# Kernel tuning notes

Hardware: AMD Instinct MI355X
Metric: run time of the kernel (lower is better)

Reference implementation:

```python
import jax, jax.numpy as jnp
import numpy as np

EPS = 1e-5

def _proj(x, W, g, b, m, v):
    # 1x1 conv (no bias) + BatchNorm2d (inference stats) + ReLU
    y = jnp.einsum('bchw,oc->bohw', x, W)
    scale = g / jnp.sqrt(v + EPS)
    y = y * scale[:, None, None] + (b - m * scale)[:, None, None]
    return jax.nn.relu(y)

def setup_inputs() -> dict:
    key = jax.random.key(0)
    B, C, H, W = 4, 192, 64, 64
    ks = jax.random.split(key, 10)
    d = {
        'lr_hsi': jax.random.normal(ks[0], (B, C, H, W), jnp.float32),
        'refine_hsi': jax.random.normal(ks[1], (B, C, H, W), jnp.float32),
    }
    for i, name in enumerate(['q', 'k', 'v', 't']):
        d['W' + name] = jax.random.normal(ks[2 + i], (C, C), jnp.float32) * 0.05
        d['g' + name] = jnp.ones((C,), jnp.float32)
        d['b' + name] = jnp.zeros((C,), jnp.float32)
        d['m' + name] = jnp.zeros((C,), jnp.float32)
        d['v' + name] = jnp.ones((C,), jnp.float32)
    return d

def reference(lr_hsi, refine_hsi,
              Wq, gq, bq, mq, vq,
              Wk, gk, bk, mk, vk,
              Wv, gv, bv, mv, vv,
              Wt, gt, bt, mt, vt):
    B, C, H, W = refine_hsi.shape
    HW = H * W
    q = _proj(refine_hsi, Wq, gq, bq, mq, vq).reshape(B, C, HW).transpose(0, 2, 1)  # [B, HWq, C]
    k = _proj(lr_hsi, Wk, gk, bk, mk, vk).reshape(B, C, HW)                          # [B, C, HWk]
    v = _proj(lr_hsi, Wv, gv, bv, mv, vv).reshape(B, C, HW).transpose(0, 2, 1)      # [B, HWk, C]
    corr = jnp.einsum('bqc,bck->bqk', q, k) * (C ** -0.5)  # [B, HWq, HWk]
    corr = jax.nn.softmax(corr, axis=1)  # NOTE: softmax over the QUERY axis (dim=1), as in source
    ss = jnp.einsum('bqk,bkc->bqc', corr, v)               # [B, HWq, C]
    ss = ss.transpose(0, 2, 1).reshape(B, C, H, W)
    out = _proj(ss, Wt, gt, bt, mt, vt)
    return (out, corr)
```

## Files before the change

### kernel.cpp

```cpp
#include <hip/hip_runtime.h>
#include <math.h>

typedef __attribute__((ext_vector_type(4))) float f32x4;
typedef __attribute__((ext_vector_type(8))) short bf16x8;

__device__ __forceinline__ unsigned short f2bf(float f) {
  unsigned int u = __builtin_bit_cast(unsigned int, f);
  u += 0x7FFFu + ((u >> 16) & 1u);
  return (unsigned short)(u >> 16);
}

__device__ __forceinline__ f32x4 mfma16(bf16x8 a, bf16x8 b, f32x4 c) {
  return __builtin_amdgcn_mfma_f32_16x16x32_bf16(a, b, c, 0, 0, 0);
}

__global__ void prep_kernel(const float* __restrict__ W, const float* __restrict__ g,
                            const float* __restrict__ bb, const float* __restrict__ mm,
                            const float* __restrict__ vv,
                            unsigned short* __restrict__ Wout, float* __restrict__ bout,
                            float alpha) {
  int idx = blockIdx.x * 256 + threadIdx.x;
  if (idx < 192 * 192) {
    int o = idx / 192;
    float s = g[o] * rsqrtf(vv[o] + 1e-5f);
    Wout[idx] = f2bf(W[idx] * s * alpha);
  }
  if (idx < 192) {
    float s = g[idx] * rsqrtf(vv[idx] + 1e-5f);
    bout[idx] = (bb[idx] - mm[idx] * s) * alpha;
  }
}

template <int LAYOUT, bool F32OUT>
__launch_bounds__(256)
__global__ void proj_kernel(const float* __restrict__ X,
                            const unsigned short* __restrict__ Wp,
                            const float* __restrict__ bias,
                            void* __restrict__ Yv) {
  const int o0 = blockIdx.x * 64;
  const int hw0 = blockIdx.y * 64;
  const int b = blockIdx.z;
  const int w = threadIdx.x >> 6, l = threadIdx.x & 63;
  const int l16 = l & 15, lg = l >> 4;
  const float* Xb = X + (size_t)b * 192 * 4096;

  f32x4 acc[4] = {f32x4{0,0,0,0}, f32x4{0,0,0,0}, f32x4{0,0,0,0}, f32x4{0,0,0,0}};

  for (int ks = 0; ks < 6; ++ks) {
    const int c0 = ks * 32 + lg * 8;
    bf16x8 a = *(const bf16x8*)(Wp + (size_t)(o0 + 16 * w + l16) * 192 + c0);
#pragma unroll
    for (int n = 0; n < 4; ++n) {
      const int hw = hw0 + 16 * n + l16;
      bf16x8 bfr;
#pragma unroll
      for (int j = 0; j < 8; ++j)
        bfr[j] = (short)f2bf(Xb[(size_t)(c0 + j) * 4096 + hw]);
      acc[n] = mfma16(a, bfr, acc[n]);
    }
  }

#pragma unroll
  for (int n = 0; n < 4; ++n) {
    const int hw = hw0 + 16 * n + l16;
    float vv4[4];
#pragma unroll
    for (int r = 0; r < 4; ++r) {
      const int o = o0 + 16 * w + lg * 4 + r;
      vv4[r] = fmaxf(acc[n][r] + bias[o], 0.0f);
    }
    if (LAYOUT == 1) {
      unsigned int lo = (unsigned)f2bf(vv4[0]) | ((unsigned)f2bf(vv4[1]) << 16);
      unsigned int hi = (unsigned)f2bf(vv4[2]) | ((unsigned)f2bf(vv4[3]) << 16);
      uint2 pk; pk.x = lo; pk.y = hi;
      *(uint2*)((unsigned short*)Yv + ((size_t)b * 4096 + hw) * 192 + o0 + 16 * w + lg * 4) = pk;
    } else {
#pragma unroll
      for (int r = 0; r < 4; ++r) {
        const int o = o0 + 16 * w + lg * 4 + r;
        if (F32OUT)
          ((float*)Yv)[((size_t)b * 192 + o) * 4096 + hw] = vv4[r];
        else
          ((unsigned short*)Yv)[((size_t)b * 192 + o) * 4096 + hw] = f2bf(vv4[r]);
      }
    }
  }
}

__launch_bounds__(256)
__global__ void pass1_kernel(const unsigned short* __restrict__ qp,
                             const unsigned short* __restrict__ kpT,
                             float* __restrict__ colsum) {
  const int q0 = blockIdx.x * 128, k0 = blockIdx.y * 128, b = blockIdx.z;
  const int w = threadIdx.x >> 6, l = threadIdx.x & 63;
  const int l16 = l & 15, lg = l >> 4;
  const unsigned short* qb = qp + (size_t)b * 4096 * 192;
  const unsigned short* kb = kpT + (size_t)b * 4096 * 192;

  __shared__ __align__(16) unsigned short kpl[128][200];
  __shared__ float cs[4][128];

  {
    const int t = threadIdx.x;
#pragma unroll
    for (int i = 0; i < 12; ++i) {
      int idx = t + i * 256;
      int row = idx / 24, cu = idx % 24;
      uint4 vdat = *(const uint4*)(kb + (size_t)(k0 + row) * 192 + cu * 8);
      *(uint4*)&kpl[row][cu * 8] = vdat;
    }
  }
  __syncthreads();

  f32x4 acc[2][8];
#pragma unroll
  for (int m = 0; m < 2; ++m)
#pragma unroll
    for (int n = 0; n < 8; ++n) acc[m][n] = f32x4{0, 0, 0, 0};

  for (int ks = 0; ks < 6; ++ks) {
    const int c0 = ks * 32 + lg * 8;
    bf16x8 a0 = *(const bf16x8*)(qb + (size_t)(q0 + 32 * w + l16) * 192 + c0);
    bf16x8 a1 = *(const bf16x8*)(qb + (size_t)(q0 + 32 * w + 16 + l16) * 192 + c0);
#pragma unroll
    for (int n = 0; n < 8; ++n) {
      bf16x8 bfr = *(const bf16x8*)&kpl[16 * n + l16][c0];
      acc[0][n] = mfma16(a0, bfr, acc[0][n]);
      acc[1][n] = mfma16(a1, bfr, acc[1][n]);
    }
  }

  float part[8];
#pragma unroll
  for (int n = 0; n < 8; ++n) {
    float s = 0.f;
#pragma unroll
    for (int r = 0; r < 4; ++r)
      s += __builtin_amdgcn_exp2f(acc[0][n][r]) + __builtin_amdgcn_exp2f(acc[1][n][r]);
    s += __shfl_xor(s, 16);
    s += __shfl_xor(s, 32);
    part[n] = s;
  }
  if (l < 16) {
#pragma unroll
    for (int n = 0; n < 8; ++n) cs[w][16 * n + l] = part[n];
  }
  __syncthreads();
  const int t = threadIdx.x;
  if (t < 128) {
    float s = cs[0][t] + cs[1][t] + cs[2][t] + cs[3][t];
    atomicAdd(&colsum[(size_t)b * 4096 + k0 + t], s);
  }
}

__global__ void invert_kernel(float* __restrict__ p, int n) {
  int i = blockIdx.x * 256 + threadIdx.x;
  if (i < n) p[i] = 1.0f / p[i];
}

__launch_bounds__(512)
__global__ void pass2_kernel(const unsigned short* __restrict__ qp,
                             const unsigned short* __restrict__ kpT,
                             const unsigned short* __restrict__ vpN,
                             const float* __restrict__ rcol,
                             float* __restrict__ corr,
                             float* __restrict__ ssN) {
  const int q0 = blockIdx.x * 64;
  const int b = blockIdx.y;
  const int w = threadIdx.x >> 6, l = threadIdx.x & 63;
  const int l16 = l & 15, lg = l >> 4;
  const int mw = w & 1, nw = w >> 1;
  const unsigned short* qb = qp + (size_t)b * 4096 * 192;
  const unsigned short* kb = kpT + (size_t)b * 4096 * 192;
  const unsigned short* vb = vpN + (size_t)b * 192 * 4096;
  const float* rc = rcol + (size_t)b * 4096;
  float* corb = corr + (size_t)b * 4096 * 4096;

  __shared__ __align__(16) float cor[64][132];

  bf16x8 af[2][6];
#pragma unroll
  for (int tm = 0; tm < 2; ++tm)
#pragma unroll
    for (int ks = 0; ks < 6; ++ks)
      af[tm][ks] = *(const bf16x8*)(qb + (size_t)(q0 + 16 * (2 * mw + tm) + l16) * 192 + ks * 32 + lg * 8);

  f32x4 ssa[2][3];
#pragma unroll
  for (int tm = 0; tm < 2; ++tm)
#pragma unroll
    for (int j = 0; j < 3; ++j) ssa[tm][j] = f32x4{0, 0, 0, 0};

  for (int kc = 0; kc < 32; ++kc) {
    const int k0 = kc * 128;
    f32x4 sa[2][2];
#pragma unroll
    for (int tm = 0; tm < 2; ++tm)
#pragma unroll
      for (int tn = 0; tn < 2; ++tn) sa[tm][tn] = f32x4{0, 0, 0, 0};

    for (int ks = 0; ks < 6; ++ks) {
      const int c0 = ks * 32 + lg * 8;
#pragma unroll
      for (int tn = 0; tn < 2; ++tn) {
        const int kcol = k0 + 16 * (2 * nw + tn) + l16;
        bf16x8 bfr = *(const bf16x8*)(kb + (size_t)kcol * 192 + c0);
        sa[0][tn] = mfma16(af[0][ks], bfr, sa[0][tn]);
        sa[1][tn] = mfma16(af[1][ks], bfr, sa[1][tn]);
      }
    }
    float rcv[2];
#pragma unroll
    for (int tn = 0; tn < 2; ++tn) rcv[tn] = rc[k0 + 16 * (2 * nw + tn) + l16];
#pragma unroll
    for (int tm = 0; tm < 2; ++tm)
#pragma unroll
      for (int tn = 0; tn < 2; ++tn)
#pragma unroll
        for (int r = 0; r < 4; ++r)
          sa[tm][tn][r] = __builtin_amdgcn_exp2f(sa[tm][tn][r]) * rcv[tn];

    __syncthreads();
#pragma unroll
    for (int tm = 0; tm < 2; ++tm)
#pragma unroll
      for (int tn = 0; tn < 2; ++tn) {
        const int col = 16 * (2 * nw + tn) + l16;
#pragma unroll
        for (int r = 0; r < 4; ++r)
          cor[16 * (2 * mw + tm) + lg * 4 + r][col] = sa[tm][tn][r];
      }
    __syncthreads();

    {
      const int t = threadIdx.x;
#pragma unroll
      for (int it = 0; it < 4; ++it) {
        int idx = t + it * 512;
        int row = idx >> 5, seg = idx & 31;
        f32x4 v4 = *(const f32x4*)&cor[row][seg * 4];
        *(f32x4*)(corb + (size_t)(q0 + row) * 4096 + k0 + seg * 4) = v4;
      }
    }

#pragma unroll
    for (int ks2 = 0; ks2 < 4; ++ks2) {
      const int cc = ks2 * 32 + lg * 8;
      bf16x8 pa[2];
#pragma unroll
      for (int tm = 0; tm < 2; ++tm) {
        f32x4 p0 = *(const f32x4*)&cor[16 * (2 * mw + tm) + l16][cc];
        f32x4 p1 = *(const f32x4*)&cor[16 * (2 * mw + tm) + l16][cc + 4];
#pragma unroll
        for (int j = 0; j < 4; ++j) {
          pa[tm][j] = (short)f2bf(p0[j]);
          pa[tm][j + 4] = (short)f2bf(p1[j]);
        }
      }
#pragma unroll
      for (int j = 0; j < 3; ++j) {
        const int ccol = 16 * (nw + 4 * j) + l16;
        bf16x8 bfr = *(const bf16x8*)(vb + (size_t)ccol * 4096 + k0 + cc);
        ssa[0][j] = mfma16(pa[0], bfr, ssa[0][j]);
        ssa[1][j] = mfma16(pa[1], bfr, ssa[1][j]);
      }
    }
  }

#pragma unroll
  for (int tm = 0; tm < 2; ++tm)
#pragma unroll
    for (int j = 0; j < 3; ++j) {
      const int ccol = 16 * (nw + 4 * j) + l16;
#pragma unroll
      for (int r = 0; r < 4; ++r) {
        const int qrow = q0 + 16 * (2 * mw + tm) + lg * 4 + r;
        ssN[((size_t)b * 192 + ccol) * 4096 + qrow] = ssa[tm][j][r];
      }
    }
}

extern "C" void kernel_launch(void* const* d_in, const int* in_sizes, int n_in,
                              void* d_out, int out_size, void* d_ws, size_t ws_size,
                              hipStream_t stream) {
  (void)in_sizes; (void)n_in; (void)out_size; (void)ws_size;
  const float* lr = (const float*)d_in[0];
  const float* refine = (const float*)d_in[1];

  char* ws = (char*)d_ws;
  unsigned short* w4 = (unsigned short*)(ws + 0);
  float* bias4 = (float*)(ws + 294912);
  unsigned short* qp = (unsigned short*)(ws + 297984);
  unsigned short* kp = (unsigned short*)(ws + 297984 + 6291456);
  unsigned short* vp = (unsigned short*)(ws + 297984 + 2 * 6291456);
  float* colsum = (float*)(ws + 297984 + 3 * 6291456);
  float* ssN = (float*)(ws + 297984 + 3 * 6291456 + 65536);

  float* out0 = (float*)d_out;
  float* corr = out0 + 3145728;

  const float alpha = (float)(1.4426950408889634 / sqrt(192.0));

  for (int p = 0; p < 4; ++p) {
    prep_kernel<<<dim3(144), dim3(256), 0, stream>>>(
        (const float*)d_in[2 + 5 * p], (const float*)d_in[3 + 5 * p],
        (const float*)d_in[4 + 5 * p], (const float*)d_in[5 + 5 * p],
        (const float*)d_in[6 + 5 * p],
        w4 + p * 36864, bias4 + p * 192, p == 0 ? alpha : 1.0f);
  }
  hipMemsetAsync(colsum, 0, 65536, stream);

  proj_kernel<1, false><<<dim3(3, 64, 4), dim3(256), 0, stream>>>(refine, w4, bias4, qp);
  proj_kernel<1, false><<<dim3(3, 64, 4), dim3(256), 0, stream>>>(lr, w4 + 36864, bias4 + 192, kp);
  proj_kernel<0, false><<<dim3(3, 64, 4), dim3(256), 0, stream>>>(lr, w4 + 2 * 36864, bias4 + 2 * 192, vp);

  pass1_kernel<<<dim3(32, 32, 4), dim3(256), 0, stream>>>(qp, kp, colsum);
  invert_kernel<<<dim3(64), dim3(256), 0, stream>>>(colsum, 16384);
  pass2_kernel<<<dim3(64, 4), dim3(512), 0, stream>>>(qp, kp, vp, colsum, corr, ssN);

  proj_kernel<0, true><<<dim3(3, 64, 4), dim3(256), 0, stream>>>(ssN, w4 + 3 * 36864, bias4 + 3 * 192, out0);
}
```

Before: 312.9 us.

## Split pass2 key range across two blocks and sum partials in final projection

```diff
diff --git a/kernel.cpp b/kernel.cpp
--- a/kernel.cpp
+++ b/kernel.cpp
@@ -31,12 +31,12 @@
   }
 }
 
-template <int LAYOUT, bool F32OUT>
+template <int LAYOUT>
 __launch_bounds__(256)
 __global__ void proj_kernel(const float* __restrict__ X,
                             const unsigned short* __restrict__ Wp,
                             const float* __restrict__ bias,
-                            void* __restrict__ Yv) {
+                            unsigned short* __restrict__ Yv) {
   const int o0 = blockIdx.x * 64;
   const int hw0 = blockIdx.y * 64;
   const int b = blockIdx.z;
@@ -73,16 +73,59 @@
       unsigned int lo = (unsigned)f2bf(vv4[0]) | ((unsigned)f2bf(vv4[1]) << 16);
       unsigned int hi = (unsigned)f2bf(vv4[2]) | ((unsigned)f2bf(vv4[3]) << 16);
       uint2 pk; pk.x = lo; pk.y = hi;
-      *(uint2*)((unsigned short*)Yv + ((size_t)b * 4096 + hw) * 192 + o0 + 16 * w + lg * 4) = pk;
+      *(uint2*)(Yv + ((size_t)b * 4096 + hw) * 192 + o0 + 16 * w + lg * 4) = pk;
     } else {
 #pragma unroll
       for (int r = 0; r < 4; ++r) {
         const int o = o0 + 16 * w + lg * 4 + r;
-        if (F32OUT)
-          ((float*)Yv)[((size_t)b * 192 + o) * 4096 + hw] = vv4[r];
-        else
-          ((unsigned short*)Yv)[((size_t)b * 192 + o) * 4096 + hw] = f2bf(vv4[r]);
-      }
+        Yv[((size_t)b * 192 + o) * 4096 + hw] = f2bf(vv4[r]);
+      }
+    }
+  }
+}
+
+template <int NS>
+__launch_bounds__(256)
+__global__ void proj_sum_kernel(const float* __restrict__ X,
+                                const unsigned short* __restrict__ Wp,
+                                const float* __restrict__ bias,
+                                float* __restrict__ Yv) {
+  const int o0 = blockIdx.x * 64;
+  const int hw0 = blockIdx.y * 64;
+  const int b = blockIdx.z;
+  const int w = threadIdx.x >> 6, l = threadIdx.x & 63;
+  const int l16 = l & 15, lg = l >> 4;
+  const float* Xb = X + (size_t)b * 192 * 4096;
+  const size_t sstride = (size_t)4 * 192 * 4096;
+
+  f32x4 acc[4] = {f32x4{0,0,0,0}, f32x4{0,0,0,0}, f32x4{0,0,0,0}, f32x4{0,0,0,0}};
+
+  for (int ks = 0; ks < 6; ++ks) {
+    const int c0 = ks * 32 + lg * 8;
+    bf16x8 a = *(const bf16x8*)(Wp + (size_t)(o0 + 16 * w + l16) * 192 + c0);
+#pragma unroll
+    for (int n = 0; n < 4; ++n) {
+      const int hw = hw0 + 16 * n + l16;
+      bf16x8 bfr;
+#pragma unroll
+      for (int j = 0; j < 8; ++j) {
+        float s = Xb[(size_t)(c0 + j) * 4096 + hw];
+#pragma unroll
+        for (int ss = 1; ss < NS; ++ss)
+          s += Xb[(size_t)(c0 + j) * 4096 + hw + ss * sstride];
+        bfr[j] = (short)f2bf(s);
+      }
+      acc[n] = mfma16(a, bfr, acc[n]);
+    }
+  }
+
+#pragma unroll
+  for (int n = 0; n < 4; ++n) {
+    const int hw = hw0 + 16 * n + l16;
+#pragma unroll
+    for (int r = 0; r < 4; ++r) {
+      const int o = o0 + 16 * w + lg * 4 + r;
+      Yv[((size_t)b * 192 + o) * 4096 + hw] = fmaxf(acc[n][r] + bias[o], 0.0f);
     }
   }
 }
@@ -158,15 +201,18 @@
   if (i < n) p[i] = 1.0f / p[i];
 }
 
+template <int NS>
 __launch_bounds__(512)
 __global__ void pass2_kernel(const unsigned short* __restrict__ qp,
                              const unsigned short* __restrict__ kpT,
                              const unsigned short* __restrict__ vpN,
                              const float* __restrict__ rcol,
                              float* __restrict__ corr,
-                             float* __restrict__ ssN) {
+                             float* __restrict__ ssP) {
   const int q0 = blockIdx.x * 64;
-  const int b = blockIdx.y;
+  const int s = blockIdx.y;
+  const int b = blockIdx.z;
+  const int kc0 = s * (32 / NS);
   const int w = threadIdx.x >> 6, l = threadIdx.x & 63;
   const int l16 = l & 15, lg = l >> 4;
   const int mw = w & 1, nw = w >> 1;
@@ -175,6 +221,7 @@
   const unsigned short* vb = vpN + (size_t)b * 192 * 4096;
   const float* rc = rcol + (size_t)b * 4096;
   float* corb = corr + (size_t)b * 4096 * 4096;
+  float* ssb = ssP + (size_t)(s * 4 + b) * 192 * 4096;
 
   __shared__ __align__(16) float cor[64][132];
 
@@ -191,7 +238,7 @@
 #pragma unroll
     for (int j = 0; j < 3; ++j) ssa[tm][j] = f32x4{0, 0, 0, 0};
 
-  for (int kc = 0; kc < 32; ++kc) {
+  for (int kc = kc0; kc < kc0 + 32 / NS; ++kc) {
     const int k0 = kc * 128;
     f32x4 sa[2][2];
 #pragma unroll
@@ -239,7 +286,7 @@
         int idx = t + it * 512;
         int row = idx >> 5, seg = idx & 31;
         f32x4 v4 = *(const f32x4*)&cor[row][seg * 4];
-        *(f32x4*)(corb + (size_t)(q0 + row) * 4096 + k0 + seg * 4) = v4;
+        __builtin_nontemporal_store(v4, (f32x4*)(corb + (size_t)(q0 + row) * 4096 + k0 + seg * 4));
       }
     }
 
@@ -275,7 +322,7 @@
 #pragma unroll
       for (int r = 0; r < 4; ++r) {
         const int qrow = q0 + 16 * (2 * mw + tm) + lg * 4 + r;
-        ssN[((size_t)b * 192 + ccol) * 4096 + qrow] = ssa[tm][j][r];
+        ssb[(size_t)ccol * 4096 + qrow] = ssa[tm][j][r];
       }
     }
 }
@@ -283,7 +330,7 @@
 extern "C" void kernel_launch(void* const* d_in, const int* in_sizes, int n_in,
                               void* d_out, int out_size, void* d_ws, size_t ws_size,
                               hipStream_t stream) {
-  (void)in_sizes; (void)n_in; (void)out_size; (void)ws_size;
+  (void)in_sizes; (void)n_in; (void)out_size;
   const float* lr = (const float*)d_in[0];
   const float* refine = (const float*)d_in[1];
 
@@ -294,7 +341,11 @@
   unsigned short* kp = (unsigned short*)(ws + 297984 + 6291456);
   unsigned short* vp = (unsigned short*)(ws + 297984 + 2 * 6291456);
   float* colsum = (float*)(ws + 297984 + 3 * 6291456);
-  float* ssN = (float*)(ws + 297984 + 3 * 6291456 + 65536);
+  float* ssP = (float*)(ws + 297984 + 3 * 6291456 + 65536);
+
+  const size_t base = 297984 + (size_t)3 * 6291456 + 65536;
+  const size_t slab = (size_t)4 * 192 * 4096 * 4;
+  int NS = (ws_size >= base + 2 * slab) ? 2 : 1;
 
   float* out0 = (float*)d_out;
   float* corr = out0 + 3145728;
@@ -310,13 +361,18 @@
   }
   hipMemsetAsync(colsum, 0, 65536, stream);
 
-  proj_kernel<1, false><<<dim3(3, 64, 4), dim3(256), 0, stream>>>(refine, w4, bias4, qp);
-  proj_kernel<1, false><<<dim3(3, 64, 4), dim3(256), 0, stream>>>(lr, w4 + 36864, bias4 + 192, kp);
-  proj_kernel<0, false><<<dim3(3, 64, 4), dim3(256), 0, stream>>>(lr, w4 + 2 * 36864, bias4 + 2 * 192, vp);
+  proj_kernel<1><<<dim3(3, 64, 4), dim3(256), 0, stream>>>(refine, w4, bias4, qp);
+  proj_kernel<1><<<dim3(3, 64, 4), dim3(256), 0, stream>>>(lr, w4 + 36864, bias4 + 192, kp);
+  proj_kernel<0><<<dim3(3, 64, 4), dim3(256), 0, stream>>>(lr, w4 + 2 * 36864, bias4 + 2 * 192, vp);
 
   pass1_kernel<<<dim3(32, 32, 4), dim3(256), 0, stream>>>(qp, kp, colsum);
   invert_kernel<<<dim3(64), dim3(256), 0, stream>>>(colsum, 16384);
-  pass2_kernel<<<dim3(64, 4), dim3(512), 0, stream>>>(qp, kp, vp, colsum, corr, ssN);
-
-  proj_kernel<0, true><<<dim3(3, 64, 4), dim3(256), 0, stream>>>(ssN, w4 + 3 * 36864, bias4 + 3 * 192, out0);
-}
+
+  if (NS == 2) {
+    pass2_kernel<2><<<dim3(64, 2, 4), dim3(512), 0, stream>>>(qp, kp, vp, colsum, corr, ssP);
+    proj_sum_kernel<2><<<dim3(3, 64, 4), dim3(256), 0, stream>>>(ssP, w4 + 3 * 36864, bias4 + 3 * 192, out0);
+  } else {
+    pass2_kernel<1><<<dim3(64, 1, 4), dim3(512), 0, stream>>>(qp, kp, vp, colsum, corr, ssP);
+    proj_sum_kernel<1><<<dim3(3, 64, 4), dim3(256), 0, stream>>>(ssP, w4 + 3 * 36864, bias4 + 3 * 192, out0);
+  }
+}
```

New measurement: 293.8 us. -6.1%, faster.
